# Kernel tuning notes

Hardware: AMD Instinct MI355X
Metric: run time of the kernel (lower is better)

The kernel has to match this reference:

```python
import jax, jax.numpy as jnp
import numpy as np


def conv1x1(x, W, b):
    # x: [B, Cin, H, W], W: [Cout, Cin], b: [Cout] -> [B, Cout, H, W]
    return jnp.einsum('bchw,oc->bohw', x, W) + b[None, :, None, None]


def setup_inputs() -> dict:
    key = jax.random.key(0)
    ks = jax.random.split(key, 8)
    B, C, H, Wd = 8, 512, 96, 96
    C8 = C // 8
    s_in = 1.0 / np.sqrt(C)
    return {
        'x': jax.random.normal(ks[0], (B, C, H, Wd), dtype=jnp.float32),
        'Wq': jax.random.normal(ks[1], (C8, C), dtype=jnp.float32) * s_in,
        'bq': jax.random.normal(ks[2], (C8,), dtype=jnp.float32) * 0.01,
        'Wk': jax.random.normal(ks[3], (C8, C), dtype=jnp.float32) * s_in,
        'bk': jax.random.normal(ks[4], (C8,), dtype=jnp.float32) * 0.01,
        'Wv': jax.random.normal(ks[5], (C, C), dtype=jnp.float32) * s_in,
        'bv': jax.random.normal(ks[6], (C,), dtype=jnp.float32) * 0.01,
        # torch init is zeros, but a nonzero gamma exercises the attention path
        'gamma': jax.random.normal(ks[7], (1,), dtype=jnp.float32) * 0.1,
    }


def reference(x, Wq, bq, Wk, bk, Wv, bv, gamma):
    # Height-axis (criss-cross H branch) self-attention, batched over (B, W).
    q = conv1x1(x, Wq, bq)   # [B, C8, H, W]
    k = conv1x1(x, Wk, bk)   # [B, C8, H, W]
    v = conv1x1(x, Wv, bv)   # [B, C,  H, W]
    # energy[b,w,i,j] = sum_c q[b,c,i,w] * k[b,c,j,w]
    energy = jnp.einsum('bciw,bcjw->bwij', q, k)
    att = jax.nn.softmax(energy, axis=-1)           # softmax over key-height j
    out = jnp.einsum('bcjw,bwij->bciw', v, att)     # [B, C, H, W]
    return gamma[0] * out + x
```

## Files before the change

### kernel.cpp

```cpp
#include <hip/hip_runtime.h>
#include <hip/hip_bf16.h>


typedef __attribute__((ext_vector_type(8))) short bh8;
typedef __attribute__((ext_vector_type(4))) float fx4;

#define MFMA16(a, b, c) __builtin_amdgcn_mfma_f32_16x16x32_bf16((a), (b), (c), 0, 0, 0)
#define MFMA8(a, b, c) __builtin_amdgcn_mfma_f32_16x16x32_fp8_fp8((a), (b), (c), 0, 0, 0)

__device__ __forceinline__ unsigned short f2bf(float f) {
  unsigned u = __float_as_uint(f);
  u += 0x7fffu + ((u >> 16) & 1u);
  return (unsigned short)(u >> 16);
}
__device__ __forceinline__ float bf2f(unsigned short u) {
  return __uint_as_float((unsigned)u << 16);
}
__device__ __forceinline__ unsigned char f2e4m3(float f) {
  unsigned b = __float_as_uint(f);
  unsigned s = (b >> 24) & 0x80u;
  unsigned a = b & 0x7fffffffu;
  float af = __uint_as_float(a);
  if (af >= 448.f) return (unsigned char)(s | 0x7e);
  if (af < 0.015625f) {
    int n = (int)(af * 512.0f + 0.5f);
    return (unsigned char)(s | (unsigned)n);
  }
  a += 0x7ffffu + ((a >> 20) & 1u);
  unsigned E = a >> 23, M = (a >> 20) & 7u;
  if (E >= 136u) return (unsigned char)(s | 0x7e);
  return (unsigned char)(s | ((E - 120u) << 3) | M);
}
#if __has_builtin(__builtin_amdgcn_cvt_pk_fp8_f32)
#define CVTPK8(a, b) __builtin_amdgcn_cvt_pk_fp8_f32((a), (b), 0, false)
#else
#define CVTPK8(a, b) ((int)f2e4m3(a) | ((int)f2e4m3(b) << 8))
#endif

__global__ __launch_bounds__(256) void prep_w(const float* __restrict__ Wq,
                                              const float* __restrict__ Wk,
                                              const float* __restrict__ Wv,
                                              short* __restrict__ wf) {
  int tid = blockIdx.x * 256 + threadIdx.x;
  if (tid >= 40960) return;
  int lane = tid & 63;
  int es = (tid >> 6) & 15;
  int gt = tid >> 10;
  int rt = lane & 15;
  int colbase = es * 32 + (lane >> 4) * 8;
  const float* src;
  size_t dst;
  if (gt < 8) {
    int m = gt * 16 + rt;
    src = (m < 64) ? (Wq + (size_t)m * 512) : (Wk + (size_t)(m - 64) * 512);
    dst = (size_t)((gt * 16 + es) * 64 + lane) * 8;
  } else {
    int ct = gt - 8;
    src = Wv + (size_t)(ct * 16 + rt) * 512;
    dst = 65536u + (size_t)((ct * 16 + es) * 64 + lane) * 8;
  }
  bh8 v;
#pragma unroll
  for (int r = 0; r < 8; ++r) v[r] = (short)f2bf(src[colbase + r]);
  *(bh8*)(wf + dst) = v;
}

__global__ __launch_bounds__(512) void transpose_in(const float* __restrict__ x,
                                                    unsigned short* __restrict__ xT) {
  __shared__ unsigned short L[96 * 132];
  int bi = blockIdx.x;
  int ct = bi & 3;
  int hb = bi >> 2;
  int h = hb % 96;
  int b = hb / 96;
  int tid = threadIdx.x;
  const float* xs = x + ((size_t)(b * 512 + ct * 128) * 96 + h) * 96;
#pragma unroll
  for (int i = 0; i < 12; ++i) {
    int idx = tid + 512 * i;
    int cc = idx / 48, wp = idx - cc * 48;
    float2 v = *(const float2*)(xs + (size_t)cc * 9216 + 2 * wp);
    L[(2 * wp) * 132 + cc] = f2bf(v.x);
    L[(2 * wp + 1) * 132 + cc] = f2bf(v.y);
  }
  __syncthreads();
  unsigned short* dst = xT + ((size_t)(b * 96) * 96 + h) * 512 + ct * 128;
#pragma unroll
  for (int i = 0; i < 6; ++i) {
    int idx = tid + 512 * i;
    int w = idx >> 5, ccq = idx & 31;
    *(ushort4*)(dst + (size_t)w * 49152 + ccq * 4) =
        *(const ushort4*)&L[w * 132 + ccq * 4];
  }
}

__global__ __launch_bounds__(512) void untrans(const unsigned short* __restrict__ oT,
                                               float* __restrict__ out, int b0) {
  __shared__ unsigned short L[128 * 101];
  int bi = blockIdx.x;
  int ct = bi & 3;
  int hb = bi >> 2;
  int h = hb % 96;
  int brel = hb / 96;
  int b = b0 + brel;
  int tid = threadIdx.x;
  const unsigned short* src = oT + ((size_t)(brel * 96) * 96 + h) * 512 + ct * 128;
#pragma unroll
  for (int i = 0; i < 3; ++i) {
    int idx = tid + 512 * i;
    int w = idx >> 4, ccb = idx & 15;
    bh8 v = *(const bh8*)(src + (size_t)w * 49152 + ccb * 8);
#pragma unroll
    for (int r = 0; r < 8; ++r) L[(ccb * 8 + r) * 101 + w] = (unsigned short)v[r];
  }
  __syncthreads();
  float* os = out + ((size_t)(b * 512 + ct * 128) * 96 + h) * 96;
#pragma unroll
  for (int i = 0; i < 12; ++i) {
    int idx = tid + 512 * i;
    int cc = idx / 48, wp = idx - cc * 48;
    float2 v;
    v.x = bf2f(L[cc * 101 + 2 * wp]);
    v.y = bf2f(L[cc * 101 + 2 * wp + 1]);
    *(float2*)(os + (size_t)cc * 9216 + 2 * wp) = v;
  }
}

#define XO5 0
#define QO5 98304
#define KO5 110592
#define AT5 122880
#define V5A 132864
#define V5B 98304
#define SMEM5 157440

__global__ __launch_bounds__(512, 2) void cc_fused7(
    const float* __restrict__ bq, const float* __restrict__ bk,
    const float* __restrict__ bv, const float* __restrict__ gamma,
    const short* __restrict__ wf, const unsigned short* __restrict__ xT,
    unsigned short* __restrict__ outTm, unsigned short* __restrict__ outT7) {
  extern __shared__ char smem[];
  const int tid = threadIdx.x;
  const int l = tid & 63, wv = tid >> 6;
  const int rl = l & 15, kg = l >> 4;
  const int bid = blockIdx.x;
  const float g0 = gamma[0];
  const unsigned short* xrow = xT + (size_t)bid * 49152;
  const int mg = wv >> 1, ng = wv & 1;

  unsigned short* obase = (bid < 672)
      ? (outTm + (size_t)bid * 49152)
      : (outT7 + (size_t)(bid - 672) * 49152);

  auto vblk = [&](int cb, int vo) {
    const int mtb = mg * 4;
    const short* wvb = wf + 65536;
    fx4 vac[4][3] = {};
    bh8 ac[4];
#pragma unroll
    for (int q = 0; q < 4; ++q)
      ac[q] = *(const bh8*)(wvb + (((cb * 16 + mtb + q) * 16 + 0) * 64 + l) * 8);
#pragma unroll 2
    for (int es = 0; es < 16; ++es) {
      int esn = (es < 15) ? es + 1 : 15;
      bh8 an[4];
#pragma unroll
      for (int q = 0; q < 4; ++q)
        an[q] = *(const bh8*)(wvb + (((cb * 16 + mtb + q) * 16 + esn) * 64 + l) * 8);
      int kb = es * 64 + kg * 16;
      __builtin_amdgcn_s_setprio(1);
#pragma unroll
      for (int t = 0; t < 3; ++t) {
        int j = (3 * ng + t) * 16 + rl;
        bh8 bx = *(const bh8*)(smem + XO5 + j * 1024 + (kb ^ ((j & 7) << 4)));
#pragma unroll
        for (int q = 0; q < 4; ++q) vac[q][t] = MFMA16(ac[q], bx, vac[q][t]);
      }
      __builtin_amdgcn_s_setprio(0);
#pragma unroll
      for (int q = 0; q < 4; ++q) ac[q] = an[q];
    }
#pragma unroll
    for (int q = 0; q < 4; ++q)
#pragma unroll
      for (int r = 0; r < 4; ++r) {
        int row = (mtb + q) * 16 + kg * 4 + r;
        int sz = ((row >> 2) & 3) << 3;
        int a = row * 96 + ng * 48 + rl;
        unsigned char* vp = (unsigned char*)smem + vo;
        int p01 = CVTPK8(vac[q][0][r], vac[q][1][r]);
        int p22 = CVTPK8(vac[q][2][r], vac[q][2][r]);
        vp[a ^ sz] = (unsigned char)p01;
        vp[(a + 16) ^ sz] = (unsigned char)(p01 >> 8);
        vp[(a + 32) ^ sz] = (unsigned char)p22;
      }
  };

  auto pv = [&](int cb, int vo) {
    const int ig = wv & 1, cg = wv >> 1;
    fx4 pac[3][4] = {};
    __builtin_amdgcn_s_setprio(1);
#pragma unroll
    for (int ks = 0; ks < 3; ++ks) {
      long aa[3], bb[4];
#pragma unroll
      for (int s = 0; s < 3; ++s)
        aa[s] = *(const long*)(smem + AT5 + ((ig * 3 + s) * 16 + rl) * 104 +
                               ks * 32 + kg * 8);
#pragma unroll
      for (int u = 0; u < 4; ++u) {
        int row = (cg * 4 + u) * 16 + rl;
        bb[u] = *(const long*)(smem + vo +
                               ((row * 96 + ks * 32 + kg * 8) ^ (((row >> 2) & 3) << 3)));
      }
#pragma unroll
      for (int s = 0; s < 3; ++s)
#pragma unroll
        for (int u = 0; u < 4; ++u) pac[s][u] = MFMA8(aa[s], bb[u], pac[s][u]);
    }
    __builtin_amdgcn_s_setprio(0);
#pragma unroll
    for (int s = 0; s < 3; ++s)
#pragma unroll
      for (int u = 0; u < 4; ++u) {
        int c = cb * 256 + (cg * 4 + u) * 16 + rl;
        float bvc = bv[c];
#pragma unroll
        for (int r = 0; r < 4; ++r) {
          int i = (ig * 3 + s) * 16 + kg * 4 + r;
          unsigned short xv = *(const unsigned short*)(
              smem + XO5 + i * 1024 + ((2 * c) ^ ((i & 7) << 4)));
          obase[(size_t)i * 512 + c] =
              f2bf(g0 * (pac[s][u][r] + bvc) + bf2f(xv));
        }
      }
  };

#pragma unroll
  for (int i = 0; i < 12; ++i) {
    int idx = tid + 512 * i;
    int j = idx >> 6, cbk = idx & 63;
    bh8 v = *(const bh8*)(xrow + (size_t)j * 512 + cbk * 8);
    *(bh8*)(smem + XO5 + j * 1024 + ((cbk * 16) ^ ((j & 7) << 4))) = v;
  }
  __syncthreads();

  {
    fx4 acc[2][3] = {};
    bh8 a0c = *(const bh8*)(wf + (((2 * mg + 0) * 16 + 0) * 64 + l) * 8);
    bh8 a1c = *(const bh8*)(wf + (((2 * mg + 1) * 16 + 0) * 64 + l) * 8);
#pragma unroll 2
    for (int es = 0; es < 16; ++es) {
      int esn = (es < 15) ? es + 1 : 15;
      bh8 a0n = *(const bh8*)(wf + (((2 * mg + 0) * 16 + esn) * 64 + l) * 8);
      bh8 a1n = *(const bh8*)(wf + (((2 * mg + 1) * 16 + esn) * 64 + l) * 8);
      int kb = es * 64 + kg * 16;
      __builtin_amdgcn_s_setprio(1);
#pragma unroll
      for (int t = 0; t < 3; ++t) {
        int j = (3 * ng + t) * 16 + rl;
        bh8 bx = *(const bh8*)(smem + XO5 + j * 1024 + (kb ^ ((j & 7) << 4)));
        acc[0][t] = MFMA16(a0c, bx, acc[0][t]);
        acc[1][t] = MFMA16(a1c, bx, acc[1][t]);
      }
      __builtin_amdgcn_s_setprio(0);
      a0c = a0n;
      a1c = a1n;
    }
#pragma unroll
    for (int q = 0; q < 2; ++q) {
      int base = (2 * mg + q) * 16;
      const float* bp = (base < 64) ? bq : bk;
      const int qko = (base < 64) ? QO5 : KO5;
      const int mb = base & 63;
#pragma unroll
      for (int r = 0; r < 4; ++r) {
        int ml = mb + kg * 4 + r;
        float bias = bp[ml];
#pragma unroll
        for (int t = 0; t < 3; ++t) {
          int i = (3 * ng + t) * 16 + rl;
          *(unsigned short*)(smem + qko + i * 128 + ((ml * 2) ^ ((i & 7) << 4))) =
              f2bf(acc[q][t][r] + bias);
        }
      }
    }
  }
  __syncthreads();

  if (wv < 6) {
    const int i0 = wv * 16;
    fx4 e[6] = {};
#pragma unroll
    for (int ks = 0; ks < 2; ++ks) {
      int kb = (ks * 32 + kg * 8) * 2;
      int ia = i0 + rl;
      bh8 aq = *(const bh8*)(smem + QO5 + ia * 128 + (kb ^ ((ia & 7) << 4)));
#pragma unroll
      for (int jt = 0; jt < 6; ++jt) {
        int j = jt * 16 + rl;
        bh8 bkf = *(const bh8*)(smem + KO5 + j * 128 + (kb ^ ((j & 7) << 4)));
        e[jt] = MFMA16(aq, bkf, e[jt]);
      }
    }
#pragma unroll
    for (int r = 0; r < 4; ++r) {
      float mx = e[0][r];
#pragma unroll
      for (int jt = 1; jt < 6; ++jt) mx = fmaxf(mx, e[jt][r]);
      mx = fmaxf(mx, __shfl_xor(mx, 1));
      mx = fmaxf(mx, __shfl_xor(mx, 2));
      mx = fmaxf(mx, __shfl_xor(mx, 4));
      mx = fmaxf(mx, __shfl_xor(mx, 8));
      float pp[6], s = 0.f;
#pragma unroll
      for (int jt = 0; jt < 6; ++jt) { pp[jt] = __expf(e[jt][r] - mx); s += pp[jt]; }
      s += __shfl_xor(s, 1);
      s += __shfl_xor(s, 2);
      s += __shfl_xor(s, 4);
      s += __shfl_xor(s, 8);
      float inv = 1.0f / s;
      int i = i0 + kg * 4 + r;
      unsigned char* arow = (unsigned char*)smem + AT5 + i * 104 + rl;
      int p01 = CVTPK8(pp[0] * inv, pp[1] * inv);
      int p23 = CVTPK8(pp[2] * inv, pp[3] * inv);
      int p45 = CVTPK8(pp[4] * inv, pp[5] * inv);
      arow[0] = (unsigned char)p01;
      arow[16] = (unsigned char)(p01 >> 8);
      arow[32] = (unsigned char)p23;
      arow[48] = (unsigned char)(p23 >> 8);
      arow[64] = (unsigned char)p45;
      arow[80] = (unsigned char)(p45 >> 8);
    }
  }
  vblk(0, V5A);
  __syncthreads();

  pv(0, V5A);
  vblk(1, V5B);
  __syncthreads();
  pv(1, V5B);
}

__global__ __launch_bounds__(512, 2) void cc_fused_legacy(
    const float* __restrict__ x, const float* __restrict__ bq,
    const float* __restrict__ bk, const float* __restrict__ bv,
    const float* __restrict__ gamma, const short* __restrict__ wf,
    float* __restrict__ out) {
  extern __shared__ char smem[];
  const int tid = threadIdx.x;
  const int l = tid & 63, wv = tid >> 6;
  const int rl = l & 15, kg = l >> 4;
  const int bid = blockIdx.x;
  const int b = (bid >> 3) / 12;
  const int w = (bid & 7) * 12 + ((bid >> 3) % 12);
  const float g0 = gamma[0];
  const float* xb = x + (size_t)b * 4718592 + w;
  for (int idx = tid; idx < 24576; idx += 512) {
    int j = idx >> 8;
    int c = (idx & 255) * 2;
    float a0 = xb[(size_t)c * 9216 + j * 96];
    float a1 = xb[(size_t)(c + 1) * 9216 + j * 96];
    unsigned pk = (unsigned)f2bf(a0) | ((unsigned)f2bf(a1) << 16);
    *(unsigned*)(smem + j * 1024 + ((c * 2) ^ ((j & 7) << 4))) = pk;
  }
  __syncthreads();
  {
    fx4 acc[6] = {};
    for (int es = 0; es < 16; ++es) {
      bh8 a = *(const bh8*)(wf + ((wv * 16 + es) * 64 + l) * 8);
      int kb = (es * 32 + kg * 8) * 2;
#pragma unroll
      for (int nt = 0; nt < 6; ++nt) {
        int j = nt * 16 + rl;
        bh8 bx = *(const bh8*)(smem + j * 1024 + (kb ^ ((j & 7) << 4)));
        acc[nt] = MFMA16(a, bx, acc[nt]);
      }
    }
    const float* bp = (wv < 4) ? bq : bk;
    const int qko = (wv < 4) ? 118272 : 130560;
    const int mb = (wv * 16) & 63;
#pragma unroll
    for (int r = 0; r < 4; ++r) {
      int ml = mb + kg * 4 + r;
      float bias = bp[ml];
#pragma unroll
      for (int nt = 0; nt < 6; ++nt) {
        int i = nt * 16 + rl;
        *(unsigned short*)(smem + qko + i * 128 + ((ml * 2) ^ ((i & 7) << 4))) =
            f2bf(acc[nt][r] + bias);
      }
    }
  }
  __syncthreads();
  if (wv < 6) {
    const int i0 = wv * 16;
    fx4 e[6] = {};
#pragma unroll
    for (int ks = 0; ks < 2; ++ks) {
      int kb = (ks * 32 + kg * 8) * 2;
      int ia = i0 + rl;
      bh8 aq = *(const bh8*)(smem + 118272 + ia * 128 + (kb ^ ((ia & 7) << 4)));
#pragma unroll
      for (int jt = 0; jt < 6; ++jt) {
        int j = jt * 16 + rl;
        bh8 bkf = *(const bh8*)(smem + 130560 + j * 128 + (kb ^ ((j & 7) << 4)));
        e[jt] = MFMA16(aq, bkf, e[jt]);
      }
    }
#pragma unroll
    for (int r = 0; r < 4; ++r) {
      float mx = e[0][r];
#pragma unroll
      for (int jt = 1; jt < 6; ++jt) mx = fmaxf(mx, e[jt][r]);
      mx = fmaxf(mx, __shfl_xor(mx, 1));
      mx = fmaxf(mx, __shfl_xor(mx, 2));
      mx = fmaxf(mx, __shfl_xor(mx, 4));
      mx = fmaxf(mx, __shfl_xor(mx, 8));
      float p[6], s = 0.f;
#pragma unroll
      for (int jt = 0; jt < 6; ++jt) { p[jt] = __expf(e[jt][r] - mx); s += p[jt]; }
      s += __shfl_xor(s, 1);
      s += __shfl_xor(s, 2);
      s += __shfl_xor(s, 4);
      s += __shfl_xor(s, 8);
      float inv = 1.0f / s;
      int i = i0 + kg * 4 + r;
#pragma unroll
      for (int jt = 0; jt < 6; ++jt) {
        int j = jt * 16 + rl;
        *(unsigned short*)(smem + 98304 + i * 208 + 2 * j) = f2bf(p[jt] * inv);
      }
    }
  }
  __syncthreads();
  for (int cb = 0; cb < 8; ++cb) {
    {
      const int mt = wv >> 1, ntb = (wv & 1) * 3;
      fx4 acc[3] = {};
      for (int es = 0; es < 16; ++es) {
        bh8 a = *(const bh8*)(wf + 65536 + (((cb * 4 + mt) * 16 + es) * 64 + l) * 8);
        int kb = (es * 32 + kg * 8) * 2;
#pragma unroll
        for (int t = 0; t < 3; ++t) {
          int j = (ntb + t) * 16 + rl;
          bh8 bx = *(const bh8*)(smem + j * 1024 + (kb ^ ((j & 7) << 4)));
          acc[t] = MFMA16(a, bx, acc[t]);
        }
      }
#pragma unroll
      for (int t = 0; t < 3; ++t) {
        int j = (ntb + t) * 16 + rl;
#pragma unroll
        for (int r = 0; r < 4; ++r) {
          int cl = mt * 16 + kg * 4 + r;
          *(unsigned short*)(smem + 118272 + cl * 208 + 2 * j) = f2bf(acc[t][r]);
        }
      }
    }
    __syncthreads();
    {
      fx4 acc[3] = {};
      const int tg0 = wv * 3;
#pragma unroll
      for (int ks = 0; ks < 3; ++ks) {
        int jb = (ks * 32 + kg * 8) * 2;
#pragma unroll
        for (int s = 0; s < 3; ++s) {
          int it = (tg0 + s) >> 2, ct = (tg0 + s) & 3;
          bh8 a = *(const bh8*)(smem + 98304 + (it * 16 + rl) * 208 + jb);
          bh8 bvv = *(const bh8*)(smem + 118272 + (ct * 16 + rl) * 208 + jb);
          acc[s] = MFMA16(a, bvv, acc[s]);
        }
      }
#pragma unroll
      for (int s = 0; s < 3; ++s) {
        int it = (tg0 + s) >> 2, ct = (tg0 + s) & 3;
        int c = cb * 64 + ct * 16 + rl;
        float bvc = bv[c];
        size_t base = (size_t)(b * 512 + c) * 9216 + w;
#pragma unroll
        for (int r = 0; r < 4; ++r) {
          int i = it * 16 + kg * 4 + r;
          size_t g = base + (size_t)i * 96;
          out[g] = g0 * (acc[s][r] + bvc) + x[g];
        }
      }
    }
    __syncthreads();
  }
}

extern "C" void kernel_launch(void* const* d_in, const int* in_sizes, int n_in,
                              void* d_out, int out_size, void* d_ws, size_t ws_size,
                              hipStream_t stream) {
  const float* x = (const float*)d_in[0];
  const float* Wq = (const float*)d_in[1];
  const float* bq = (const float*)d_in[2];
  const float* Wk = (const float*)d_in[3];
  const float* bk = (const float*)d_in[4];
  const float* Wv = (const float*)d_in[5];
  const float* bv = (const float*)d_in[6];
  const float* gamma = (const float*)d_in[7];
  float* out = (float*)d_out;
  short* wf = (short*)d_ws;

  prep_w<<<160, 256, 0, stream>>>(Wq, Wk, Wv, wf);

  const size_t WS_SMALL = 1048576u + 9437184u;
  const size_t WS_BIG = 1048576u + 75497472u;

  if (ws_size >= WS_SMALL) {
    unsigned short* xT = (unsigned short*)d_out;

    hipFuncSetAttribute((const void*)cc_fused7,
                        hipFuncAttributeMaxDynamicSharedMemorySize, SMEM5);
    transpose_in<<<3072, 512, 0, stream>>>(x, xT);

    if (ws_size >= WS_BIG) {
      unsigned short* outTall = (unsigned short*)((char*)d_ws + 1048576);
      cc_fused7<<<768, 512, SMEM5, stream>>>(bq, bk, bv, gamma, (const short*)wf,
                                             xT, outTall,
                                             outTall + (size_t)672 * 49152);
      untrans<<<3072, 512, 0, stream>>>(outTall, out, 0);
    } else {
      unsigned short* outTm = (unsigned short*)((char*)d_out + 75497472);
      unsigned short* outT7 = (unsigned short*)((char*)d_ws + 1048576);
      cc_fused7<<<768, 512, SMEM5, stream>>>(bq, bk, bv, gamma, (const short*)wf,
                                             xT, outTm, outT7);
      untrans<<<1536, 512, 0, stream>>>(outTm, out, 0);
      untrans<<<768, 512, 0, stream>>>(outTm + (size_t)4 * 4718592, out, 4);
      untrans<<<384, 512, 0, stream>>>(outTm + (size_t)6 * 4718592, out, 6);
      untrans<<<384, 512, 0, stream>>>(outT7, out, 7);
    }
  } else {
    hipFuncSetAttribute((const void*)cc_fused_legacy,
                        hipFuncAttributeMaxDynamicSharedMemorySize, 142848);
    cc_fused_legacy<<<768, 512, 142848, stream>>>(x, bq, bk, bv, gamma,
                                                  (const short*)wf, out);
  }
}
```

Measured before the change: 166.7 us.

## Fuse first V-projection block into the QK projection loop sharing x fragments

Computes the first 256-channel block of the V projection inside the same K-loop that computes Q and K, reusing each loaded x fragment from shared memory for six MFMAs instead of two. The separate vblk(0) pass and its reread of x tiles are removed, and the V results are packed to fp8 directly into the V5A buffer. This raises accumulator register pressure (12 extra fx4 accumulators plus 4 prefetched weight fragments), which could reduce occupancy or cause spills under the 512x2 launch bounds.

```diff
diff --git a/kernel.cpp b/kernel.cpp
--- a/kernel.cpp
+++ b/kernel.cpp
@@ -134,7 +134,7 @@
 #define V5B 98304
 #define SMEM5 157440
 
-__global__ __launch_bounds__(512, 2) void cc_fused7(
+__global__ __launch_bounds__(512, 2) void cc_fused8(
     const float* __restrict__ bq, const float* __restrict__ bk,
     const float* __restrict__ bv, const float* __restrict__ gamma,
     const short* __restrict__ wf, const unsigned short* __restrict__ xT,
@@ -246,26 +246,37 @@
   __syncthreads();
 
   {
+    const int mtb = mg * 4;
+    const short* wvb = wf + 65536;
+    fx4 vac[4][3] = {};
     fx4 acc[2][3] = {};
-    bh8 a0c = *(const bh8*)(wf + (((2 * mg + 0) * 16 + 0) * 64 + l) * 8);
-    bh8 a1c = *(const bh8*)(wf + (((2 * mg + 1) * 16 + 0) * 64 + l) * 8);
+    bh8 ac[4];
+#pragma unroll
+    for (int q = 0; q < 4; ++q)
+      ac[q] = *(const bh8*)(wvb + (((mtb + q) * 16 + 0) * 64 + l) * 8);
 #pragma unroll 2
     for (int es = 0; es < 16; ++es) {
       int esn = (es < 15) ? es + 1 : 15;
-      bh8 a0n = *(const bh8*)(wf + (((2 * mg + 0) * 16 + esn) * 64 + l) * 8);
-      bh8 a1n = *(const bh8*)(wf + (((2 * mg + 1) * 16 + esn) * 64 + l) * 8);
+      bh8 an[4];
+#pragma unroll
+      for (int q = 0; q < 4; ++q)
+        an[q] = *(const bh8*)(wvb + (((mtb + q) * 16 + esn) * 64 + l) * 8);
+      bh8 p0 = *(const bh8*)(wf + (((2 * mg + 0) * 16 + es) * 64 + l) * 8);
+      bh8 p1 = *(const bh8*)(wf + (((2 * mg + 1) * 16 + es) * 64 + l) * 8);
       int kb = es * 64 + kg * 16;
       __builtin_amdgcn_s_setprio(1);
 #pragma unroll
       for (int t = 0; t < 3; ++t) {
         int j = (3 * ng + t) * 16 + rl;
         bh8 bx = *(const bh8*)(smem + XO5 + j * 1024 + (kb ^ ((j & 7) << 4)));
-        acc[0][t] = MFMA16(a0c, bx, acc[0][t]);
-        acc[1][t] = MFMA16(a1c, bx, acc[1][t]);
+        acc[0][t] = MFMA16(p0, bx, acc[0][t]);
+        acc[1][t] = MFMA16(p1, bx, acc[1][t]);
+#pragma unroll
+        for (int q = 0; q < 4; ++q) vac[q][t] = MFMA16(ac[q], bx, vac[q][t]);
       }
       __builtin_amdgcn_s_setprio(0);
-      a0c = a0n;
-      a1c = a1n;
+#pragma unroll
+      for (int q = 0; q < 4; ++q) ac[q] = an[q];
     }
 #pragma unroll
     for (int q = 0; q < 2; ++q) {
@@ -285,6 +296,20 @@
         }
       }
     }
+#pragma unroll
+    for (int q = 0; q < 4; ++q)
+#pragma unroll
+      for (int r = 0; r < 4; ++r) {
+        int row = (mtb + q) * 16 + kg * 4 + r;
+        int sz = ((row >> 2) & 3) << 3;
+        int a = row * 96 + ng * 48 + rl;
+        unsigned char* vp = (unsigned char*)smem + V5A;
+        int p01 = CVTPK8(vac[q][0][r], vac[q][1][r]);
+        int p22 = CVTPK8(vac[q][2][r], vac[q][2][r]);
+        vp[a ^ sz] = (unsigned char)p01;
+        vp[(a + 16) ^ sz] = (unsigned char)(p01 >> 8);
+        vp[(a + 32) ^ sz] = (unsigned char)p22;
+      }
   }
   __syncthreads();
 
@@ -333,12 +358,12 @@
       arow[80] = (unsigned char)(p45 >> 8);
     }
   }
-  vblk(0, V5A);
   __syncthreads();
 
   pv(0, V5A);
   vblk(1, V5B);
   __syncthreads();
+
   pv(1, V5B);
 }
 
@@ -513,20 +538,20 @@
   if (ws_size >= WS_SMALL) {
     unsigned short* xT = (unsigned short*)d_out;
 
-    hipFuncSetAttribute((const void*)cc_fused7,
+    hipFuncSetAttribute((const void*)cc_fused8,
                         hipFuncAttributeMaxDynamicSharedMemorySize, SMEM5);
     transpose_in<<<3072, 512, 0, stream>>>(x, xT);
 
     if (ws_size >= WS_BIG) {
       unsigned short* outTall = (unsigned short*)((char*)d_ws + 1048576);
-      cc_fused7<<<768, 512, SMEM5, stream>>>(bq, bk, bv, gamma, (const short*)wf,
+      cc_fused8<<<768, 512, SMEM5, stream>>>(bq, bk, bv, gamma, (const short*)wf,
                                              xT, outTall,
                                              outTall + (size_t)672 * 49152);
       untrans<<<3072, 512, 0, stream>>>(outTall, out, 0);
     } else {
       unsigned short* outTm = (unsigned short*)((char*)d_out + 75497472);
       unsigned short* outT7 = (unsigned short*)((char*)d_ws + 1048576);
-      cc_fused7<<<768, 512, SMEM5, stream>>>(bq, bk, bv, gamma, (const short*)wf,
+      cc_fused8<<<768, 512, SMEM5, stream>>>(bq, bk, bv, gamma, (const short*)wf,
                                              xT, outTm, outT7);
       untrans<<<1536, 512, 0, stream>>>(outTm, out, 0);
       untrans<<<768, 512, 0, stream>>>(outTm + (size_t)4 * 4718592, out, 4);
```

New measurement: 167.0 us. Within noise of the previous version (+0.2%).

## Double block to 1024 threads, halving per-wave tiles in fused attention kernel

Applied to the files above, without the earlier changes.

The fused kernel now launches 16 waves per block instead of 8. Each wave computes half as many output tiles in the Q/K projection, the V projection and the PV product, and the input staging loop is redistributed over the wider block. The aim is more resident waves per CU to hide LDS and MFMA latency, since shared memory already limits residency to one block per CU. In exchange, the launch bounds of (1024, 4) ask for far more waves than the LDS allows, which may cap registers tightly and cause spills. Each wave also does less work between barriers.

```diff
diff --git a/kernel.cpp b/kernel.cpp
--- a/kernel.cpp
+++ b/kernel.cpp
@@ -134,7 +134,7 @@
 #define V5B 98304
 #define SMEM5 157440
 
-__global__ __launch_bounds__(512, 2) void cc_fused7(
+__global__ __launch_bounds__(1024, 4) void cc_fused9(
     const float* __restrict__ bq, const float* __restrict__ bk,
     const float* __restrict__ bv, const float* __restrict__ gamma,
     const short* __restrict__ wf, const unsigned short* __restrict__ xT,
@@ -153,19 +153,19 @@
       : (outT7 + (size_t)(bid - 672) * 49152);
 
   auto vblk = [&](int cb, int vo) {
-    const int mtb = mg * 4;
+    const int mtb = mg * 2;
     const short* wvb = wf + 65536;
-    fx4 vac[4][3] = {};
-    bh8 ac[4];
-#pragma unroll
-    for (int q = 0; q < 4; ++q)
+    fx4 vac[2][3] = {};
+    bh8 ac[2];
+#pragma unroll
+    for (int q = 0; q < 2; ++q)
       ac[q] = *(const bh8*)(wvb + (((cb * 16 + mtb + q) * 16 + 0) * 64 + l) * 8);
 #pragma unroll 2
     for (int es = 0; es < 16; ++es) {
       int esn = (es < 15) ? es + 1 : 15;
-      bh8 an[4];
-#pragma unroll
-      for (int q = 0; q < 4; ++q)
+      bh8 an[2];
+#pragma unroll
+      for (int q = 0; q < 2; ++q)
         an[q] = *(const bh8*)(wvb + (((cb * 16 + mtb + q) * 16 + esn) * 64 + l) * 8);
       int kb = es * 64 + kg * 16;
       __builtin_amdgcn_s_setprio(1);
@@ -173,15 +173,15 @@
       for (int t = 0; t < 3; ++t) {
         int j = (3 * ng + t) * 16 + rl;
         bh8 bx = *(const bh8*)(smem + XO5 + j * 1024 + (kb ^ ((j & 7) << 4)));
-#pragma unroll
-        for (int q = 0; q < 4; ++q) vac[q][t] = MFMA16(ac[q], bx, vac[q][t]);
+        vac[0][t] = MFMA16(ac[0], bx, vac[0][t]);
+        vac[1][t] = MFMA16(ac[1], bx, vac[1][t]);
       }
       __builtin_amdgcn_s_setprio(0);
-#pragma unroll
-      for (int q = 0; q < 4; ++q) ac[q] = an[q];
-    }
-#pragma unroll
-    for (int q = 0; q < 4; ++q)
+      ac[0] = an[0];
+      ac[1] = an[1];
+    }
+#pragma unroll
+    for (int q = 0; q < 2; ++q)
 #pragma unroll
       for (int r = 0; r < 4; ++r) {
         int row = (mtb + q) * 16 + kg * 4 + r;
@@ -198,32 +198,32 @@
 
   auto pv = [&](int cb, int vo) {
     const int ig = wv & 1, cg = wv >> 1;
-    fx4 pac[3][4] = {};
+    fx4 pac[3][2] = {};
     __builtin_amdgcn_s_setprio(1);
 #pragma unroll
     for (int ks = 0; ks < 3; ++ks) {
-      long aa[3], bb[4];
+      long aa[3], bb[2];
 #pragma unroll
       for (int s = 0; s < 3; ++s)
         aa[s] = *(const long*)(smem + AT5 + ((ig * 3 + s) * 16 + rl) * 104 +
                                ks * 32 + kg * 8);
 #pragma unroll
-      for (int u = 0; u < 4; ++u) {
-        int row = (cg * 4 + u) * 16 + rl;
+      for (int u = 0; u < 2; ++u) {
+        int row = (cg * 2 + u) * 16 + rl;
         bb[u] = *(const long*)(smem + vo +
                                ((row * 96 + ks * 32 + kg * 8) ^ (((row >> 2) & 3) << 3)));
       }
 #pragma unroll
       for (int s = 0; s < 3; ++s)
 #pragma unroll
-        for (int u = 0; u < 4; ++u) pac[s][u] = MFMA8(aa[s], bb[u], pac[s][u]);
+        for (int u = 0; u < 2; ++u) pac[s][u] = MFMA8(aa[s], bb[u], pac[s][u]);
     }
     __builtin_amdgcn_s_setprio(0);
 #pragma unroll
     for (int s = 0; s < 3; ++s)
 #pragma unroll
-      for (int u = 0; u < 4; ++u) {
-        int c = cb * 256 + (cg * 4 + u) * 16 + rl;
+      for (int u = 0; u < 2; ++u) {
+        int c = cb * 256 + (cg * 2 + u) * 16 + rl;
         float bvc = bv[c];
 #pragma unroll
         for (int r = 0; r < 4; ++r) {
@@ -237,8 +237,8 @@
   };
 
 #pragma unroll
-  for (int i = 0; i < 12; ++i) {
-    int idx = tid + 512 * i;
+  for (int i = 0; i < 6; ++i) {
+    int idx = tid + 1024 * i;
     int j = idx >> 6, cbk = idx & 63;
     bh8 v = *(const bh8*)(xrow + (size_t)j * 512 + cbk * 8);
     *(bh8*)(smem + XO5 + j * 1024 + ((cbk * 16) ^ ((j & 7) << 4))) = v;
@@ -246,30 +246,25 @@
   __syncthreads();
 
   {
-    fx4 acc[2][3] = {};
-    bh8 a0c = *(const bh8*)(wf + (((2 * mg + 0) * 16 + 0) * 64 + l) * 8);
-    bh8 a1c = *(const bh8*)(wf + (((2 * mg + 1) * 16 + 0) * 64 + l) * 8);
+    fx4 acc[3] = {};
+    bh8 a0c = *(const bh8*)(wf + ((mg * 16 + 0) * 64 + l) * 8);
 #pragma unroll 2
     for (int es = 0; es < 16; ++es) {
       int esn = (es < 15) ? es + 1 : 15;
-      bh8 a0n = *(const bh8*)(wf + (((2 * mg + 0) * 16 + esn) * 64 + l) * 8);
-      bh8 a1n = *(const bh8*)(wf + (((2 * mg + 1) * 16 + esn) * 64 + l) * 8);
+      bh8 a0n = *(const bh8*)(wf + ((mg * 16 + esn) * 64 + l) * 8);
       int kb = es * 64 + kg * 16;
       __builtin_amdgcn_s_setprio(1);
 #pragma unroll
       for (int t = 0; t < 3; ++t) {
         int j = (3 * ng + t) * 16 + rl;
         bh8 bx = *(const bh8*)(smem + XO5 + j * 1024 + (kb ^ ((j & 7) << 4)));
-        acc[0][t] = MFMA16(a0c, bx, acc[0][t]);
-        acc[1][t] = MFMA16(a1c, bx, acc[1][t]);
+        acc[t] = MFMA16(a0c, bx, acc[t]);
       }
       __builtin_amdgcn_s_setprio(0);
       a0c = a0n;
-      a1c = a1n;
-    }
-#pragma unroll
-    for (int q = 0; q < 2; ++q) {
-      int base = (2 * mg + q) * 16;
+    }
+    {
+      int base = mg * 16;
       const float* bp = (base < 64) ? bq : bk;
       const int qko = (base < 64) ? QO5 : KO5;
       const int mb = base & 63;
@@ -281,7 +276,7 @@
         for (int t = 0; t < 3; ++t) {
           int i = (3 * ng + t) * 16 + rl;
           *(unsigned short*)(smem + qko + i * 128 + ((ml * 2) ^ ((i & 7) << 4))) =
-              f2bf(acc[q][t][r] + bias);
+              f2bf(acc[t][r] + bias);
         }
       }
     }
@@ -339,6 +334,7 @@
   pv(0, V5A);
   vblk(1, V5B);
   __syncthreads();
+
   pv(1, V5B);
 }
 
@@ -513,21 +509,21 @@
   if (ws_size >= WS_SMALL) {
     unsigned short* xT = (unsigned short*)d_out;
 
-    hipFuncSetAttribute((const void*)cc_fused7,
+    hipFuncSetAttribute((const void*)cc_fused9,
                         hipFuncAttributeMaxDynamicSharedMemorySize, SMEM5);
     transpose_in<<<3072, 512, 0, stream>>>(x, xT);
 
     if (ws_size >= WS_BIG) {
       unsigned short* outTall = (unsigned short*)((char*)d_ws + 1048576);
-      cc_fused7<<<768, 512, SMEM5, stream>>>(bq, bk, bv, gamma, (const short*)wf,
-                                             xT, outTall,
-                                             outTall + (size_t)672 * 49152);
+      cc_fused9<<<768, 1024, SMEM5, stream>>>(bq, bk, bv, gamma, (const short*)wf,
+                                              xT, outTall,
+                                              outTall + (size_t)672 * 49152);
       untrans<<<3072, 512, 0, stream>>>(outTall, out, 0);
     } else {
       unsigned short* outTm = (unsigned short*)((char*)d_out + 75497472);
       unsigned short* outT7 = (unsigned short*)((char*)d_ws + 1048576);
-      cc_fused7<<<768, 512, SMEM5, stream>>>(bq, bk, bv, gamma, (const short*)wf,
-                                             xT, outTm, outT7);
+      cc_fused9<<<768, 1024, SMEM5, stream>>>(bq, bk, bv, gamma, (const short*)wf,
+                                              xT, outTm, outT7);
       untrans<<<1536, 512, 0, stream>>>(outTm, out, 0);
       untrans<<<768, 512, 0, stream>>>(outTm + (size_t)4 * 4718592, out, 4);
       untrans<<<384, 512, 0, stream>>>(outTm + (size_t)6 * 4718592, out, 6);
```

Result: slower. 172.9 us (+3.7%).
